# Kernel optimization log

Hardware: AMD Instinct MI355X
Metric: run time of the kernel (lower is better)

## Reference

```python
import jax, jax.numpy as jnp
import numpy as np

M = 2048
K = 512


def setup_inputs() -> dict:
    key = jax.random.key(0)
    k1, k2, k3, k4, k5 = jax.random.split(key, 5)
    inputs = jax.random.normal(k1, (16384, M), dtype=jnp.float32)
    # MyLinear(m, k): weight [k, m], bias [k] (torch Linear convention)
    s1 = 1.0 / np.sqrt(M)
    s2 = 1.0 / np.sqrt(K)
    W1 = jax.random.uniform(k2, (K, M), jnp.float32, -s1, s1)
    b1 = jax.random.uniform(k3, (K,), jnp.float32, -s1, s1)
    W2 = jax.random.uniform(k4, (M, K), jnp.float32, -s2, s2)
    b2 = jax.random.uniform(k5, (M,), jnp.float32, -s2, s2)
    return {"inputs": inputs, "W1": W1, "b1": b1, "W2": W2, "b2": b2}


def reference(inputs, W1, b1, W2, b2):
    # Original loops per sample; math is identical to one batched chain:
    # hidden = x @ W1^T + b1 ; out = hidden @ W2^T + b2 (no nonlinearity)
    hidden = jnp.einsum("bm,km->bk", inputs, W1) + b1  # [B, K]
    out = jnp.einsum("bk,mk->bm", hidden, W2) + b2     # [B, M]
    return out
```

## Files before the change

kernel.cpp:

```cpp
#include <hip/hip_runtime.h>
#include <hip/hip_bf16.h>
#include <stdint.h>


typedef short bf16x8 __attribute__((ext_vector_type(8)));
typedef float f32x4 __attribute__((ext_vector_type(4)));

static __device__ __forceinline__ unsigned short f32_to_bf16_rne(float f) {
    unsigned int u = __float_as_uint(f);
    u += 0x7fffu + ((u >> 16) & 1u);
    return (unsigned short)(u >> 16);
}

static __device__ __forceinline__ unsigned int cvt_pk_bf16(float lo, float hi) {
    unsigned int r;
    asm("v_cvt_pk_bf16_f32 %0, %1, %2" : "=v"(r) : "v"(lo), "v"(hi));
    return r;
}

__global__ void cast_weights_bf16(const float* __restrict__ w1,
                                  unsigned short* __restrict__ o1,
                                  const float* __restrict__ w2,
                                  unsigned short* __restrict__ o2, int n4each) {
    int stride = gridDim.x * blockDim.x;
    for (int i = blockIdx.x * blockDim.x + threadIdx.x; i < 2 * n4each;
         i += stride) {
        const float* in = (i < n4each) ? w1 : w2;
        unsigned short* out = (i < n4each) ? o1 : o2;
        int j = (i < n4each) ? i : i - n4each;
        float4 v = ((const float4*)in)[j];
        ushort4 o;
        o.x = f32_to_bf16_rne(v.x);
        o.y = f32_to_bf16_rne(v.y);
        o.z = f32_to_bf16_rne(v.z);
        o.w = f32_to_bf16_rne(v.w);
        ((ushort4*)out)[j] = o;
    }
}

#define GLOAD_LDS16(gsrc, ldst)                                              \
    __builtin_amdgcn_global_load_lds(                                        \
        (const __attribute__((address_space(1))) void*)(gsrc),               \
        (__attribute__((address_space(3))) void*)(ldst), 16, 0, 0)

__global__ __launch_bounds__(512, 4)
void gemm1_xcast(const float* __restrict__ X,
                 const unsigned short* __restrict__ W1,
                 const float* __restrict__ b1,
                 unsigned short* __restrict__ H) {
    constexpr int K = 2048, N = 512, BK = 64, NSTEP = K / BK;

    __shared__ __align__(16) unsigned short ldsX[2][128 * BK];
    __shared__ __align__(16) unsigned short ldsW[2][128 * BK];

    const int tid  = threadIdx.x;
    const int lane = tid & 63;
    const int wid  = tid >> 6;
    const int wr   = wid >> 2;
    const int wc   = wid & 3;

    const int bid = blockIdx.x;
    const int swz = ((bid & 7) << 6) + (bid >> 3);
    const int bm  = swz >> 2;
    const int bn  = swz & 3;
    const int brow = bm << 7;
    const int bcol = bn << 7;

    const int lrow = lane & 15;
    const int ku   = lane >> 4;
    const int rx   = lrow & 7;

    const int xrow = tid >> 2;
    const int xu0  = (tid & 3) << 1;
    const float* xptr = X + (size_t)(brow + xrow) * K + (xu0 << 3);
    const int xb0 = xrow * 128 + ((xu0 ^ (xrow & 7)) << 4);
    const int xb1 = xrow * 128 + (((xu0 | 1) ^ (xrow & 7)) << 4);

    const int wrow0 = tid >> 3;
    const int wu    = tid & 7;

    f32x4 acc[4][2] = {};
    f32x4 xv[4];

    auto loadX = [&](int k0) {
        const float* p = xptr + k0;
        xv[0] = *(const f32x4*)p;
        xv[1] = *(const f32x4*)(p + 4);
        xv[2] = *(const f32x4*)(p + 8);
        xv[3] = *(const f32x4*)(p + 12);
    };
    auto writeX = [&](unsigned short* bufX) {
        uint4 a, b;
        a.x = cvt_pk_bf16(xv[0][0], xv[0][1]);
        a.y = cvt_pk_bf16(xv[0][2], xv[0][3]);
        a.z = cvt_pk_bf16(xv[1][0], xv[1][1]);
        a.w = cvt_pk_bf16(xv[1][2], xv[1][3]);
        b.x = cvt_pk_bf16(xv[2][0], xv[2][1]);
        b.y = cvt_pk_bf16(xv[2][2], xv[2][3]);
        b.z = cvt_pk_bf16(xv[3][0], xv[3][1]);
        b.w = cvt_pk_bf16(xv[3][2], xv[3][3]);
        *(uint4*)((char*)bufX + xb0) = a;
        *(uint4*)((char*)bufX + xb1) = b;
    };
    auto stageW = [&](int k0, unsigned short* bufW) {
#pragma unroll
        for (int i = 0; i < 2; ++i) {
            const int row = i * 64 + wrow0;
            const char* src = (const char*)(W1 + (size_t)(bcol + row) * K + k0)
                              + ((wu ^ (row & 7)) << 4);
            GLOAD_LDS16(src, (char*)bufW + i * 8192 + tid * 16);
        }
    };
    auto compute = [&](const unsigned short* bufX, const unsigned short* bufW) {
#pragma unroll
        for (int kk = 0; kk < 2; ++kk) {
            const int un = ((ku + (kk << 2)) ^ rx) << 4;
            bf16x8 a[4], b[2];
#pragma unroll
            for (int m = 0; m < 4; ++m)
                a[m] = *(const bf16x8*)((const char*)bufX +
                       ((wr << 6) + (m << 4) + lrow) * 128 + un);
#pragma unroll
            for (int n = 0; n < 2; ++n)
                b[n] = *(const bf16x8*)((const char*)bufW +
                       ((wc << 5) + (n << 4) + lrow) * 128 + un);
#pragma unroll
            for (int m = 0; m < 4; ++m)
#pragma unroll
                for (int n = 0; n < 2; ++n)
                    acc[m][n] = __builtin_amdgcn_mfma_f32_16x16x32_bf16(
                        a[m], b[n], acc[m][n], 0, 0, 0);
        }
    };

    loadX(0);
    stageW(0, ldsW[0]);
    writeX(ldsX[0]);
    __syncthreads();

#pragma unroll 1
    for (int t = 0; t < NSTEP; t += 2) {
        loadX((t + 1) * BK);
        stageW((t + 1) * BK, ldsW[1]);
        compute(ldsX[0], ldsW[0]);
        writeX(ldsX[1]);
        __syncthreads();

        const bool more = (t + 2 < NSTEP);
        if (more) {
            loadX((t + 2) * BK);
            stageW((t + 2) * BK, ldsW[0]);
        }
        compute(ldsX[1], ldsW[1]);
        if (more) writeX(ldsX[0]);
        __syncthreads();
    }

    const int r0 = (lane >> 4) << 2;
#pragma unroll
    for (int n = 0; n < 2; ++n) {
        const int col = bcol + (wc << 5) + (n << 4) + lrow;
        const float bb = b1[col];
#pragma unroll
        for (int m = 0; m < 4; ++m)
#pragma unroll
            for (int j = 0; j < 4; ++j) {
                const int row = brow + (wr << 6) + (m << 4) + r0 + j;
                H[(size_t)row * N + col] = f32_to_bf16_rne(acc[m][n][j] + bb);
            }
    }
}

__global__ __launch_bounds__(256)
void gemm2(const unsigned short* __restrict__ A,
           const unsigned short* __restrict__ Bt,
           const float* __restrict__ bias,
           float* __restrict__ C) {
    constexpr int N = 2048, Kd = 512, BK = 64, NSTEP = Kd / BK;

    __shared__ __align__(16) unsigned short ldsA[128 * BK];
    __shared__ __align__(16) unsigned short ldsB[128 * BK];

    const int tid  = threadIdx.x;
    const int lane = tid & 63;
    const int wid  = tid >> 6;
    const int wr   = wid >> 1;
    const int wc   = wid & 1;

    const int bid = blockIdx.x;
    const int swz = ((bid & 7) << 8) + (bid >> 3);
    const int bn  = swz & 15;
    const int bm  = swz >> 4;
    const int brow = bm << 7;
    const int bcol = bn << 7;

    const int lrow = lane & 15;
    const int ku   = lane >> 4;
    const int rx   = lrow & 7;

    const int srow = tid >> 3;
    const int sgu  = (tid & 7) ^ (srow & 7);

    f32x4 acc[4][4] = {};

    auto stage = [&](int k0) {
#pragma unroll
        for (int i = 0; i < 4; ++i) {
            const int row = i * 32 + srow;
            const char* sa =
                (const char*)(A + (size_t)(brow + row) * Kd + k0) + (sgu << 4);
            const char* sb =
                (const char*)(Bt + (size_t)(bcol + row) * Kd + k0) + (sgu << 4);
            GLOAD_LDS16(sa, (char*)ldsA + i * 4096 + tid * 16);
            GLOAD_LDS16(sb, (char*)ldsB + i * 4096 + tid * 16);
        }
    };
    auto compute = [&]() {
#pragma unroll
        for (int kk = 0; kk < 2; ++kk) {
            const int un = ((ku + (kk << 2)) ^ rx) << 4;
            bf16x8 a[4], b[4];
#pragma unroll
            for (int m = 0; m < 4; ++m)
                a[m] = *(const bf16x8*)((const char*)ldsA +
                       ((wr << 6) + (m << 4) + lrow) * 128 + un);
#pragma unroll
            for (int n = 0; n < 4; ++n)
                b[n] = *(const bf16x8*)((const char*)ldsB +
                       ((wc << 6) + (n << 4) + lrow) * 128 + un);
#pragma unroll
            for (int m = 0; m < 4; ++m)
#pragma unroll
                for (int n = 0; n < 4; ++n)
                    acc[m][n] = __builtin_amdgcn_mfma_f32_16x16x32_bf16(
                        a[m], b[n], acc[m][n], 0, 0, 0);
        }
    };

    stage(0);
    __syncthreads();

    for (int t = 0; t < NSTEP; ++t) {
        compute();
        if (t + 1 < NSTEP) {
            __syncthreads();
            stage((t + 1) * BK);
            __syncthreads();
        }
    }

    const int r0 = (lane >> 4) << 2;
#pragma unroll
    for (int n = 0; n < 4; ++n) {
        const int col = bcol + (wc << 6) + (n << 4) + lrow;
        const float bb = bias[col];
#pragma unroll
        for (int m = 0; m < 4; ++m)
#pragma unroll
            for (int j = 0; j < 4; ++j) {
                const int row = brow + (wr << 6) + (m << 4) + r0 + j;
                C[(size_t)row * N + col] = acc[m][n][j] + bb;
            }
    }
}

extern "C" void kernel_launch(void* const* d_in, const int* in_sizes, int n_in,
                              void* d_out, int out_size, void* d_ws, size_t ws_size,
                              hipStream_t stream) {
    const float* X  = (const float*)d_in[0];
    const float* W1 = (const float*)d_in[1];
    const float* b1 = (const float*)d_in[2];
    const float* W2 = (const float*)d_in[3];
    const float* b2 = (const float*)d_in[4];

    const int B = 16384, M = 2048, Kd = 512;

    char* ws = (char*)d_ws;
    unsigned short* W1bf = (unsigned short*)ws;
    unsigned short* W2bf = W1bf + (size_t)Kd * M;
    unsigned short* Hbf  = W2bf + (size_t)M * Kd;

    cast_weights_bf16<<<2048, 256, 0, stream>>>(W1, W1bf, W2, W2bf,
                                                Kd * M / 4);

    gemm1_xcast<<<(B / 128) * (Kd / 128), 512, 0, stream>>>(X, W1bf, b1, Hbf);
    gemm2<<<(B / 128) * (M / 128), 256, 0, stream>>>(Hbf, W2bf, b2,
                                                     (float*)d_out);
}
```

Measured before the change: 133.2 us.

## Prefetch X two stages ahead and stage W through registers in GEMM1

The first GEMM kernel stops using direct global-to-LDS loads for W1. W1 tiles are now loaded into registers and written to LDS with the same swizzle as X. X prefetch is deepened to two k-steps ahead using double register buffers, and the block barrier is replaced by an explicit LDS waitcnt plus s_barrier wrapped in sched_barriers. MFMA sections are also bracketed with s_setprio to favour matrix issue. This is meant to hide more global-load latency, at the cost of extra VGPRs and possible occupancy loss.

```diff
diff --git a/kernel.cpp b/kernel.cpp
--- a/kernel.cpp
+++ b/kernel.cpp
@@ -16,6 +16,13 @@
     unsigned int r;
     asm("v_cvt_pk_bf16_f32 %0, %1, %2" : "=v"(r) : "v"(lo), "v"(hi));
     return r;
+}
+
+static __device__ __forceinline__ void block_sync_lds() {
+    asm volatile("s_waitcnt lgkmcnt(0)" ::: "memory");
+    __builtin_amdgcn_sched_barrier(0);
+    __builtin_amdgcn_s_barrier();
+    __builtin_amdgcn_sched_barrier(0);
 }
 
 __global__ void cast_weights_bf16(const float* __restrict__ w1,
@@ -70,26 +77,30 @@
     const int ku   = lane >> 4;
     const int rx   = lrow & 7;
 
-    const int xrow = tid >> 2;
-    const int xu0  = (tid & 3) << 1;
-    const float* xptr = X + (size_t)(brow + xrow) * K + (xu0 << 3);
-    const int xb0 = xrow * 128 + ((xu0 ^ (xrow & 7)) << 4);
-    const int xb1 = xrow * 128 + (((xu0 | 1) ^ (xrow & 7)) << 4);
-
-    const int wrow0 = tid >> 3;
-    const int wu    = tid & 7;
+    const int srow = tid >> 2;
+    const int su0  = (tid & 3) << 1;
+    const float* xbase = X + (size_t)(brow + srow) * K + (su0 << 3);
+    const char*  wbase = (const char*)(W1 + (size_t)(bcol + srow) * K) + (su0 << 4);
+    const int b0 = srow * 128 + ((su0 ^ (srow & 7)) << 4);
+    const int b1o = b0 ^ 16;
 
     f32x4 acc[4][2] = {};
-    f32x4 xv[4];
-
-    auto loadX = [&](int k0) {
-        const float* p = xptr + k0;
+    f32x4 xvA[4], xvB[4];
+    uint4 wv0, wv1;
+
+    auto loadX = [&](int k0, f32x4* xv) {
+        const float* p = xbase + k0;
         xv[0] = *(const f32x4*)p;
         xv[1] = *(const f32x4*)(p + 4);
         xv[2] = *(const f32x4*)(p + 8);
         xv[3] = *(const f32x4*)(p + 12);
     };
-    auto writeX = [&](unsigned short* bufX) {
+    auto loadW = [&](int k0) {
+        const char* p = wbase + (size_t)k0 * 2;
+        wv0 = *(const uint4*)p;
+        wv1 = *(const uint4*)(p + 16);
+    };
+    auto writeX = [&](const f32x4* xv, unsigned short* bufX) {
         uint4 a, b;
         a.x = cvt_pk_bf16(xv[0][0], xv[0][1]);
         a.y = cvt_pk_bf16(xv[0][2], xv[0][3]);
@@ -99,17 +110,12 @@
         b.y = cvt_pk_bf16(xv[2][2], xv[2][3]);
         b.z = cvt_pk_bf16(xv[3][0], xv[3][1]);
         b.w = cvt_pk_bf16(xv[3][2], xv[3][3]);
-        *(uint4*)((char*)bufX + xb0) = a;
-        *(uint4*)((char*)bufX + xb1) = b;
-    };
-    auto stageW = [&](int k0, unsigned short* bufW) {
-#pragma unroll
-        for (int i = 0; i < 2; ++i) {
-            const int row = i * 64 + wrow0;
-            const char* src = (const char*)(W1 + (size_t)(bcol + row) * K + k0)
-                              + ((wu ^ (row & 7)) << 4);
-            GLOAD_LDS16(src, (char*)bufW + i * 8192 + tid * 16);
-        }
+        *(uint4*)((char*)bufX + b0)  = a;
+        *(uint4*)((char*)bufX + b1o) = b;
+    };
+    auto writeW = [&](unsigned short* bufW) {
+        *(uint4*)((char*)bufW + b0)  = wv0;
+        *(uint4*)((char*)bufW + b1o) = wv1;
     };
     auto compute = [&](const unsigned short* bufX, const unsigned short* bufW) {
 #pragma unroll
@@ -124,36 +130,43 @@
             for (int n = 0; n < 2; ++n)
                 b[n] = *(const bf16x8*)((const char*)bufW +
                        ((wc << 5) + (n << 4) + lrow) * 128 + un);
+            __builtin_amdgcn_s_setprio(1);
 #pragma unroll
             for (int m = 0; m < 4; ++m)
 #pragma unroll
                 for (int n = 0; n < 2; ++n)
                     acc[m][n] = __builtin_amdgcn_mfma_f32_16x16x32_bf16(
                         a[m], b[n], acc[m][n], 0, 0, 0);
-        }
-    };
-
-    loadX(0);
-    stageW(0, ldsW[0]);
-    writeX(ldsX[0]);
-    __syncthreads();
+            __builtin_amdgcn_s_setprio(0);
+        }
+    };
+
+    loadW(0);
+    loadX(0, xvA);
+    writeW(ldsW[0]);
+    writeX(xvA, ldsX[0]);
+    loadX(BK, xvA);
+    block_sync_lds();
 
 #pragma unroll 1
     for (int t = 0; t < NSTEP; t += 2) {
-        loadX((t + 1) * BK);
-        stageW((t + 1) * BK, ldsW[1]);
+        if (t + 2 < NSTEP) loadX((t + 2) * BK, xvB);
+        loadW((t + 1) * BK);
         compute(ldsX[0], ldsW[0]);
-        writeX(ldsX[1]);
-        __syncthreads();
-
-        const bool more = (t + 2 < NSTEP);
-        if (more) {
-            loadX((t + 2) * BK);
-            stageW((t + 2) * BK, ldsW[0]);
-        }
+        writeX(xvA, ldsX[1]);
+        writeW(ldsW[1]);
+        block_sync_lds();
+
+        const bool m2 = (t + 3 < NSTEP);
+        const bool m1 = (t + 2 < NSTEP);
+        if (m2) loadX((t + 3) * BK, xvA);
+        if (m1) loadW((t + 2) * BK);
         compute(ldsX[1], ldsW[1]);
-        if (more) writeX(ldsX[0]);
-        __syncthreads();
+        if (m1) {
+            writeX(xvB, ldsX[0]);
+            writeW(ldsW[0]);
+        }
+        block_sync_lds();
     }
 
     const int r0 = (lane >> 4) << 2;
```

Measured after the change: 136.6 us. 1.02x slower.
